# Kernel optimization log

Hardware: AMD Instinct MI355X
Metric: run time of the kernel (lower is better)

Reference implementation:

```python
import jax, jax.numpy as jnp
import numpy as np

N = 50000
E = 800000
D_IN, D_HID, D_OUT = 128, 128, 64


def setup_inputs() -> dict:
    key = jax.random.key(0)
    ks = jax.random.split(key, 8)
    x = jax.random.normal(ks[0], (N, D_IN), dtype=jnp.float32)
    edge_index = jax.random.randint(ks[1], (2, E), 0, N, dtype=jnp.int64)
    # Glorot-ish init for GCNConv linear weights + zero bias (PyG default bias=True)
    def lin(k, din, dout):
        s = 1.0 / np.sqrt(din)
        return jax.random.uniform(k, (din, dout), jnp.float32, -s, s)
    return {
        "x": x,
        "edge_index": edge_index,
        "W1": lin(ks[2], D_IN, D_HID), "b1": jnp.zeros((D_HID,), jnp.float32),
        "W2": lin(ks[3], D_HID, D_HID), "b2": jnp.zeros((D_HID,), jnp.float32),
        "W3": lin(ks[4], D_HID, D_OUT), "b3": jnp.zeros((D_OUT,), jnp.float32),
    }


def _prep_edges(edge_index, n):
    # add self loops (PyG GCNConv default add_self_loops=True)
    loop = jnp.arange(n, dtype=edge_index.dtype)
    src = jnp.concatenate([edge_index[0], loop])
    dst = jnp.concatenate([edge_index[1], loop])
    deg = jax.ops.segment_sum(jnp.ones_like(dst, dtype=jnp.float32), dst, num_segments=n)
    dinv = jnp.where(deg > 0, jax.lax.rsqrt(deg), 0.0)
    norm = dinv[src] * dinv[dst]  # symmetric normalization per edge
    return src, dst, norm


def _gcn_conv(h, W, b, src, dst, norm, n):
    h = h @ W                                   # [N, dout]
    msg = h[src] * norm[:, None]                # [E+N, dout] gather
    out = jax.ops.segment_sum(msg, dst, num_segments=n)  # scatter-add
    return out + b


def reference(x, edge_index, W1, b1, W2, b2, W3, b3):
    src, dst, norm = _prep_edges(edge_index, N)
    h = jax.nn.relu(_gcn_conv(x, W1, b1, src, dst, norm, N))
    h = jax.nn.relu(_gcn_conv(h, W2, b2, src, dst, norm, N))
    return _gcn_conv(h, W3, b3, src, dst, norm, N)  # eval mode: dropout is identity
```

## Files before the change

kernel.cpp:

```cpp
#include <hip/hip_runtime.h>
#include <hip/hip_fp16.h>
#include <math.h>

#define NN 50000
#define NE 800000
#define RAWSTRIDE 96
#define NBUCK 196
#define NBBIN 196
#define BCAP 4608
#define ACH 4096
#define G1B 782
#define G2B 1563

using bf8v = __attribute__((ext_vector_type(8))) short;
using f4v  = __attribute__((ext_vector_type(4))) float;

__device__ inline unsigned short f2bf(float f) {
    unsigned int u = __float_as_uint(f);
    u += 0x7FFFu + ((u >> 16) & 1u);
    return (unsigned short)(u >> 16);
}
__device__ inline float bflo(unsigned int d) { return __uint_as_float(d << 16); }
__device__ inline float bfhi(unsigned int d) { return __uint_as_float(d & 0xFFFF0000u); }


__global__ __launch_bounds__(256) void prep_kernel(const float* __restrict__ W1,
                                                   const float* __restrict__ W2,
                                                   unsigned int* __restrict__ w1p,
                                                   unsigned int* __restrict__ w2p,
                                                   int* __restrict__ gcursor) {
    int id = blockIdx.x * 256 + threadIdx.x;
    int m = id >> 13;
    int rest = id & 8191;
    int n = rest >> 6;
    int kp = rest & 63;
    int k = kp * 2;
    const float* W = m ? W2 : W1;
    unsigned int* o = m ? w2p : w1p;
    unsigned int p = (unsigned int)f2bf(W[k * 128 + n]) |
                     ((unsigned int)f2bf(W[(k + 1) * 128 + n]) << 16);
    o[n * 64 + kp] = p;
    if (id < NBUCK) gcursor[id] = 0;
}


__device__ __forceinline__ void bin_body(const int* __restrict__ src,
                                         const int* __restrict__ dst,
                                         int* __restrict__ gcursor,
                                         unsigned int* __restrict__ bst,
                                         int bx, char* shc) {
    unsigned int* items = (unsigned int*)shc;
    int* cnt    = (int*)(shc + 16384);
    int* pref   = (int*)(shc + 17408);
    int* gstart = (int*)(shc + 18436);
    const int t = threadIdx.x;
    cnt[t] = 0;
    __syncthreads();
    const int base = bx * ACH;

    unsigned int my[16]; int myb[16], myr[16];
    #pragma unroll
    for (int i = 0; i < 16; ++i) {
        int e = base + i * 256 + t;
        my[i] = 0; myb[i] = -1; myr[i] = 0;
        if (e < NE) {
            int d = dst[e], s = src[e];
            my[i] = (unsigned int)s | ((unsigned int)d << 16);
            int b = d >> 8;
            myb[i] = b;
            myr[i] = atomicAdd(&cnt[b], 1);
        }
    }
    __syncthreads();
    if (t == 0) {
        int run = 0;
        for (int b = 0; b < 256; ++b) { pref[b] = run; run += cnt[b]; }
        pref[256] = run;
    }
    __syncthreads();
    if (cnt[t] > 0) gstart[t] = atomicAdd(&gcursor[t], cnt[t]);
    __syncthreads();
    #pragma unroll
    for (int i = 0; i < 16; ++i)
        if (myb[i] >= 0) items[pref[myb[i]] + myr[i]] = my[i];
    __syncthreads();
    const int total = pref[256];
    for (int i = t; i < total; i += 256) {
        int lo = 0, hi = 255;
        while (lo < hi) { int mid = (lo + hi + 1) >> 1; if (pref[mid] <= i) lo = mid; else hi = mid - 1; }
        int idx = gstart[lo] + (i - pref[lo]);
        if (idx < BCAP) bst[(size_t)lo * BCAP + idx] = items[i];
    }
}


__global__ __launch_bounds__(512) void sortb_kernel(const int* __restrict__ gcursor,
                                                    const unsigned int* __restrict__ bst,
                                                    int* __restrict__ cnt_g,
                                                    float* __restrict__ dinv,
                                                    unsigned short* __restrict__ raw) {
    __shared__ unsigned int items[BCAP];
    __shared__ int cnt[256], pref[257], cur[256];
    __shared__ unsigned short outl[BCAP];
    const int b = blockIdx.x;
    const int t = threadIdx.x;
    int n = gcursor[b];
    if (n > BCAP) n = BCAP;
    if (t < 256) { cnt[t] = 0; cur[t] = 0; }
    __syncthreads();
    for (int i = t; i < n; i += 512) {
        unsigned int u = bst[(size_t)b * BCAP + i];
        items[i] = u;
        atomicAdd(&cnt[(u >> 16) & 255], 1);
    }
    __syncthreads();
    if (t == 0) {
        int run = 0;
        for (int j = 0; j < 256; ++j) { pref[j] = run; run += cnt[j]; }
        pref[256] = run;
    }
    __syncthreads();
    for (int i = t; i < n; i += 512) {
        unsigned int u = items[i];
        int ln = (u >> 16) & 255;
        int r = atomicAdd(&cur[ln], 1);
        outl[pref[ln] + r] = (unsigned short)(u & 0xFFFFu);
    }
    __syncthreads();
    for (int i = t; i < n; i += 512) {
        int lo = 0, hi = 255;
        while (lo < hi) { int mid = (lo + hi + 1) >> 1; if (pref[mid] <= i) lo = mid; else hi = mid - 1; }
        int r = i - pref[lo];
        if (r < RAWSTRIDE) raw[(size_t)(b * 256 + lo) * RAWSTRIDE + r] = outl[i];
    }
    if (t < 256) {
        int node = b * 256 + t;
        if (node < NN) {
            int c = cnt[t];
            cnt_g[node] = c;
            dinv[node] = rsqrtf((float)(1 + c));
        }
    }
}


__device__ __forceinline__ void gemm128_body_f32(const float* __restrict__ A,
                                                 const unsigned short* __restrict__ Wbf,
                                                 unsigned short* __restrict__ out,
                                                 int bx, char* shc) {
    unsigned short* Dt = (unsigned short*)shc;
    const int t = threadIdx.x;
    const int row0 = bx * 64;
    const int wave = t >> 6;
    const int l64  = t & 63;
    const int m16  = l64 & 15;
    const int quad = l64 >> 4;
    const int arow = row0 + wave * 16 + m16;
    const int arowc = (arow < NN) ? arow : 0;

    f4v acc[8];
    #pragma unroll
    for (int i = 0; i < 8; ++i) acc[i] = (f4v)(0.0f);

    #pragma unroll
    for (int k0 = 0; k0 < 128; k0 += 32) {
        bf8v afrag;
        const float4* ap = (const float4*)(A + (size_t)arowc * 128 + k0 + quad * 8);
        float4 a0 = ap[0], a1 = ap[1];
        afrag[0] = (short)f2bf(a0.x); afrag[1] = (short)f2bf(a0.y);
        afrag[2] = (short)f2bf(a0.z); afrag[3] = (short)f2bf(a0.w);
        afrag[4] = (short)f2bf(a1.x); afrag[5] = (short)f2bf(a1.y);
        afrag[6] = (short)f2bf(a1.z); afrag[7] = (short)f2bf(a1.w);
        #pragma unroll
        for (int nt = 0; nt < 8; ++nt) {
            bf8v bfrag = *(const bf8v*)(Wbf + (nt * 16 + m16) * 128 + k0 + quad * 8);
            acc[nt] = __builtin_amdgcn_mfma_f32_16x16x32_bf16(afrag, bfrag, acc[nt], 0, 0, 0);
        }
    }

    #pragma unroll
    for (int nt = 0; nt < 8; ++nt) {
        #pragma unroll
        for (int r = 0; r < 4; ++r) {
            Dt[(wave * 16 + quad * 4 + r) * 136 + nt * 16 + m16] = f2bf(acc[nt][r]);
        }
    }
    __syncthreads();

    #pragma unroll
    for (int j = 0; j < 4; ++j) {
        int idx = j * 256 + t;
        int r = idx >> 4, c4 = idx & 15;
        int gr = row0 + r;
        if (gr < NN)
            ((uint4*)(out + (size_t)gr * 128))[c4] = ((const uint4*)&Dt[r * 136])[c4];
    }
}

__global__ __launch_bounds__(256) void bin_g1_kernel(const int* __restrict__ src,
                                                     const int* __restrict__ dst,
                                                     int* __restrict__ gcursor,
                                                     unsigned int* __restrict__ bst,
                                                     const float* __restrict__ x,
                                                     const unsigned short* __restrict__ w1bf,
                                                     unsigned short* __restrict__ hb) {
    __shared__ __align__(16) char sh[19472];
    if (blockIdx.x < NBBIN) {
        bin_body(src, dst, gcursor, bst, blockIdx.x, sh);
    } else {
        gemm128_body_f32(x, w1bf, hb, blockIdx.x - NBBIN, sh);
    }
}


#define ACC8(G, W_) \
    acc[0] += W_ * bflo(G.x); acc[1] += W_ * bfhi(G.x); \
    acc[2] += W_ * bflo(G.y); acc[3] += W_ * bfhi(G.y); \
    acc[4] += W_ * bflo(G.z); acc[5] += W_ * bfhi(G.z); \
    acc[6] += W_ * bflo(G.w); acc[7] += W_ * bfhi(G.w);

#define AGG128_BODY(HV, RROW, C, DIW, LANE)                                         \
    {                                                                               \
        uint4 g = HV[(size_t)wid * 16 + (LANE)];                                    \
        float ws = (DIW) * (DIW);                                                   \
        acc[0] = ws * bflo(g.x); acc[1] = ws * bfhi(g.x);                           \
        acc[2] = ws * bflo(g.y); acc[3] = ws * bfhi(g.y);                           \
        acc[4] = ws * bflo(g.z); acc[5] = ws * bfhi(g.z);                           \
        acc[6] = ws * bflo(g.w); acc[7] = ws * bfhi(g.w);                           \
    }                                                                               \
    const int cfull = (C) & ~7;                                                     \
    uint4 q;                                                                        \
    if (cfull > 0) q = *(const uint4*)(RROW);                                       \
    for (int e = 0; e < cfull; e += 8) {                                            \
        uint4 qc = q;                                                               \
        if (e + 8 < cfull) q = *(const uint4*)((RROW) + e + 8);                     \
        int c0 = qc.x & 0xFFFFu, c1 = qc.x >> 16;                                   \
        int c2 = qc.y & 0xFFFFu, c3 = qc.y >> 16;                                   \
        int c4 = qc.z & 0xFFFFu, c5 = qc.z >> 16;                                   \
        int c6 = qc.w & 0xFFFFu, c7 = qc.w >> 16;                                   \
        uint4 g0 = HV[(size_t)c0 * 16 + (LANE)];                                    \
        uint4 g1 = HV[(size_t)c1 * 16 + (LANE)];                                    \
        uint4 g2 = HV[(size_t)c2 * 16 + (LANE)];                                    \
        uint4 g3 = HV[(size_t)c3 * 16 + (LANE)];                                    \
        uint4 g4 = HV[(size_t)c4 * 16 + (LANE)];                                    \
        uint4 g5 = HV[(size_t)c5 * 16 + (LANE)];                                    \
        uint4 g6 = HV[(size_t)c6 * 16 + (LANE)];                                    \
        uint4 g7 = HV[(size_t)c7 * 16 + (LANE)];                                    \
        float w0 = (DIW) * dinv[c0], w1 = (DIW) * dinv[c1];                         \
        float w2 = (DIW) * dinv[c2], w3 = (DIW) * dinv[c3];                         \
        float w4 = (DIW) * dinv[c4], w5 = (DIW) * dinv[c5];                         \
        float w6 = (DIW) * dinv[c6], w7 = (DIW) * dinv[c7];                         \
        ACC8(g0, w0) ACC8(g1, w1) ACC8(g2, w2) ACC8(g3, w3)                         \
        ACC8(g4, w4) ACC8(g5, w5) ACC8(g6, w6) ACC8(g7, w7)                         \
    }                                                                               \
    if ((C) & 7) {                                                                  \
        int e = cfull, rem = (C) - e;                                               \
        uint4 qc = *(const uint4*)((RROW) + e);                                     \
        int c0 = qc.x & 0xFFFFu, c1 = qc.x >> 16;                                   \
        int c2 = qc.y & 0xFFFFu, c3 = qc.y >> 16;                                   \
        int c4 = qc.z & 0xFFFFu, c5 = qc.z >> 16;                                   \
        int c6 = qc.w & 0xFFFFu, c7 = qc.w >> 16;                                   \
        if (rem <= 1) c1 = 0; if (rem <= 2) c2 = 0; if (rem <= 3) c3 = 0;           \
        if (rem <= 4) c4 = 0; if (rem <= 5) c5 = 0; if (rem <= 6) c6 = 0;           \
        c7 = 0;                                                                     \
        float w0 = (DIW) * dinv[c0];                                                \
        float w1 = (rem > 1) ? (DIW) * dinv[c1] : 0.f;                              \
        float w2 = (rem > 2) ? (DIW) * dinv[c2] : 0.f;                              \
        float w3 = (rem > 3) ? (DIW) * dinv[c3] : 0.f;                              \
        float w4 = (rem > 4) ? (DIW) * dinv[c4] : 0.f;                              \
        float w5 = (rem > 5) ? (DIW) * dinv[c5] : 0.f;                              \
        float w6 = (rem > 6) ? (DIW) * dinv[c6] : 0.f;                              \
        float w7 = 0.f;                                                             \
        uint4 g0 = HV[(size_t)c0 * 16 + (LANE)];                                    \
        uint4 g1 = HV[(size_t)c1 * 16 + (LANE)];                                    \
        uint4 g2 = HV[(size_t)c2 * 16 + (LANE)];                                    \
        uint4 g3 = HV[(size_t)c3 * 16 + (LANE)];                                    \
        uint4 g4 = HV[(size_t)c4 * 16 + (LANE)];                                    \
        uint4 g5 = HV[(size_t)c5 * 16 + (LANE)];                                    \
        uint4 g6 = HV[(size_t)c6 * 16 + (LANE)];                                    \
        uint4 g7 = HV[(size_t)c7 * 16 + (LANE)];                                    \
        ACC8(g0, w0) ACC8(g1, w1) ACC8(g2, w2) ACC8(g3, w3)                         \
        ACC8(g4, w4) ACC8(g5, w5) ACC8(g6, w6) ACC8(g7, w7)                         \
    }


__global__ __launch_bounds__(256) void aggW2_kernel(const unsigned short* __restrict__ hin,
                                                    const unsigned short* __restrict__ raw,
                                                    const int* __restrict__ cnt_g,
                                                    const float* __restrict__ dinv,
                                                    const float* __restrict__ bias,
                                                    const unsigned short* __restrict__ Wbf,
                                                    unsigned short* __restrict__ out) {
    __shared__ unsigned short Zt[32 * 136];
    const int t = threadIdx.x;
    const int row0 = blockIdx.x * 32;
    const int group = t >> 4;
    const int lane  = t & 15;
    const uint4* hv = (const uint4*)hin;
    const float4* bp = (const float4*)bias;
    float4 bv0 = bp[lane * 2], bv1 = bp[lane * 2 + 1];

    for (int r = 0; r < 2; ++r) {
        const int wid = row0 + r * 16 + group;
        uint4 o = make_uint4(0u, 0u, 0u, 0u);
        if (wid < NN) {
            int c = cnt_g[wid];
            if (c > RAWSTRIDE) c = RAWSTRIDE;
            const float diw = dinv[wid];
            const unsigned short* rrow = raw + (size_t)wid * RAWSTRIDE;
            float acc[8];
            AGG128_BODY(hv, rrow, c, diw, lane)
            acc[0] += bv0.x; acc[1] += bv0.y; acc[2] += bv0.z; acc[3] += bv0.w;
            acc[4] += bv1.x; acc[5] += bv1.y; acc[6] += bv1.z; acc[7] += bv1.w;
            #pragma unroll
            for (int j = 0; j < 8; ++j) acc[j] = fmaxf(acc[j], 0.f);
            o.x = (unsigned int)f2bf(acc[0]) | ((unsigned int)f2bf(acc[1]) << 16);
            o.y = (unsigned int)f2bf(acc[2]) | ((unsigned int)f2bf(acc[3]) << 16);
            o.z = (unsigned int)f2bf(acc[4]) | ((unsigned int)f2bf(acc[5]) << 16);
            o.w = (unsigned int)f2bf(acc[6]) | ((unsigned int)f2bf(acc[7]) << 16);
        }
        *(uint4*)&Zt[(r * 16 + group) * 136 + lane * 8] = o;
    }
    __syncthreads();

    const int wave = t >> 6;
    const int l64  = t & 63;
    const int m16  = l64 & 15;
    const int quad = l64 >> 4;
    const int rh = wave & 1;
    const int nh = wave >> 1;

    f4v acc[4];
    #pragma unroll
    for (int i = 0; i < 4; ++i) acc[i] = (f4v)(0.0f);

    #pragma unroll
    for (int k0 = 0; k0 < 128; k0 += 32) {
        bf8v afrag = *(const bf8v*)&Zt[(rh * 16 + m16) * 136 + k0 + quad * 8];
        #pragma unroll
        for (int j = 0; j < 4; ++j) {
            int nt = nh * 4 + j;
            bf8v bfrag = *(const bf8v*)(Wbf + (nt * 16 + m16) * 128 + k0 + quad * 8);
            acc[j] = __builtin_amdgcn_mfma_f32_16x16x32_bf16(afrag, bfrag, acc[j], 0, 0, 0);
        }
    }
    __syncthreads();

    #pragma unroll
    for (int j = 0; j < 4; ++j) {
        #pragma unroll
        for (int rr = 0; rr < 4; ++rr) {
            Zt[(rh * 16 + quad * 4 + rr) * 136 + (nh * 4 + j) * 16 + m16] = f2bf(acc[j][rr]);
        }
    }
    __syncthreads();

    #pragma unroll
    for (int jj = 0; jj < 2; ++jj) {
        int idx = jj * 256 + t;
        int r = idx >> 4, c4 = idx & 15;
        int gr = row0 + r;
        if (gr < NN)
            ((uint4*)(out + (size_t)gr * 128))[c4] = ((const uint4*)&Zt[r * 136])[c4];
    }
}


__global__ __launch_bounds__(256) void aggG3_kernel(const unsigned short* __restrict__ hin,
                                                    const unsigned short* __restrict__ raw,
                                                    const int* __restrict__ cnt_g,
                                                    const float* __restrict__ dinv,
                                                    const float* __restrict__ bias,
                                                    const float* __restrict__ W,
                                                    unsigned short* __restrict__ outh) {
    __shared__ unsigned short Zt[32 * 136];
    const int t = threadIdx.x;
    const int row0 = blockIdx.x * 32;
    const int group = t >> 4;
    const int lane  = t & 15;
    const uint4* hv = (const uint4*)hin;
    const float4* bp = (const float4*)bias;
    float4 bv0 = bp[lane * 2], bv1 = bp[lane * 2 + 1];

    for (int r = 0; r < 2; ++r) {
        const int wid = row0 + r * 16 + group;
        uint4 o = make_uint4(0u, 0u, 0u, 0u);
        if (wid < NN) {
            int c = cnt_g[wid];
            if (c > RAWSTRIDE) c = RAWSTRIDE;
            const float diw = dinv[wid];
            const unsigned short* rrow = raw + (size_t)wid * RAWSTRIDE;
            float acc[8];
            AGG128_BODY(hv, rrow, c, diw, lane)
            acc[0] += bv0.x; acc[1] += bv0.y; acc[2] += bv0.z; acc[3] += bv0.w;
            acc[4] += bv1.x; acc[5] += bv1.y; acc[6] += bv1.z; acc[7] += bv1.w;
            #pragma unroll
            for (int j = 0; j < 8; ++j) acc[j] = fmaxf(acc[j], 0.f);
            o.x = (unsigned int)f2bf(acc[0]) | ((unsigned int)f2bf(acc[1]) << 16);
            o.y = (unsigned int)f2bf(acc[2]) | ((unsigned int)f2bf(acc[3]) << 16);
            o.z = (unsigned int)f2bf(acc[4]) | ((unsigned int)f2bf(acc[5]) << 16);
            o.w = (unsigned int)f2bf(acc[6]) | ((unsigned int)f2bf(acc[7]) << 16);
        }
        *(uint4*)&Zt[(r * 16 + group) * 136 + lane * 8] = o;
    }
    __syncthreads();

    const int cg = t & 15;
    const int rt = t >> 4;
    const float4* Wv = (const float4*)W;
    float4 acc[2];
    acc[0] = make_float4(0.f, 0.f, 0.f, 0.f);
    acc[1] = make_float4(0.f, 0.f, 0.f, 0.f);

    for (int k0 = 0; k0 < 128; k0 += 4) {
        float4 w0 = Wv[(k0 + 0) * 16 + cg];
        float4 w1 = Wv[(k0 + 1) * 16 + cg];
        float4 w2 = Wv[(k0 + 2) * 16 + cg];
        float4 w3 = Wv[(k0 + 3) * 16 + cg];
        #pragma unroll
        for (int i = 0; i < 2; ++i) {
            uint2 u = *(const uint2*)&Zt[(rt * 2 + i) * 136 + k0];
            float ax = bflo(u.x), ay = bfhi(u.x), az = bflo(u.y), aw = bfhi(u.y);
            acc[i].x += ax * w0.x + ay * w1.x + az * w2.x + aw * w3.x;
            acc[i].y += ax * w0.y + ay * w1.y + az * w2.y + aw * w3.y;
            acc[i].z += ax * w0.z + ay * w1.z + az * w2.z + aw * w3.z;
            acc[i].w += ax * w0.w + ay * w1.w + az * w2.w + aw * w3.w;
        }
    }

    #pragma unroll
    for (int i = 0; i < 2; ++i) {
        int gr = row0 + rt * 2 + i;
        if (gr < NN) {
            uint2 o;
            o.x = (unsigned int)f2bf(acc[i].x) | ((unsigned int)f2bf(acc[i].y) << 16);
            o.y = (unsigned int)f2bf(acc[i].z) | ((unsigned int)f2bf(acc[i].w) << 16);
            ((uint2*)(outh + (size_t)gr * 64))[cg] = o;
        }
    }
}


__global__ __launch_bounds__(256) void agg3_kernel(const unsigned short* __restrict__ hin,
                                                   const unsigned short* __restrict__ raw,
                                                   const int* __restrict__ cnt_g,
                                                   const float* __restrict__ dinv,
                                                   const float* __restrict__ bias,
                                                   float* __restrict__ out) {
    const int t = threadIdx.x;
    const int group = t >> 3;
    const int lane  = t & 7;
    const int wid = blockIdx.x * 32 + group;
    if (wid >= NN) return;

    int c = cnt_g[wid];
    if (c > RAWSTRIDE) c = RAWSTRIDE;
    const float diw = dinv[wid];
    const unsigned short* rrow = raw + (size_t)wid * RAWSTRIDE;
    const uint4* hv = (const uint4*)hin;

    float acc[8];
    {
        uint4 g = hv[(size_t)wid * 8 + lane];
        float ws = diw * diw;
        acc[0] = ws * bflo(g.x); acc[1] = ws * bfhi(g.x);
        acc[2] = ws * bflo(g.y); acc[3] = ws * bfhi(g.y);
        acc[4] = ws * bflo(g.z); acc[5] = ws * bfhi(g.z);
        acc[6] = ws * bflo(g.w); acc[7] = ws * bfhi(g.w);
    }

    const int cfull = c & ~7;
    uint4 q;
    if (cfull > 0) q = *(const uint4*)(rrow);
    for (int e = 0; e < cfull; e += 8) {
        uint4 qc = q;
        if (e + 8 < cfull) q = *(const uint4*)(rrow + e + 8);
        int c0 = qc.x & 0xFFFFu, c1 = qc.x >> 16;
        int c2 = qc.y & 0xFFFFu, c3 = qc.y >> 16;
        int c4 = qc.z & 0xFFFFu, c5 = qc.z >> 16;
        int c6 = qc.w & 0xFFFFu, c7 = qc.w >> 16;
        uint4 g0 = hv[(size_t)c0 * 8 + lane];
        uint4 g1 = hv[(size_t)c1 * 8 + lane];
        uint4 g2 = hv[(size_t)c2 * 8 + lane];
        uint4 g3 = hv[(size_t)c3 * 8 + lane];
        uint4 g4 = hv[(size_t)c4 * 8 + lane];
        uint4 g5 = hv[(size_t)c5 * 8 + lane];
        uint4 g6 = hv[(size_t)c6 * 8 + lane];
        uint4 g7 = hv[(size_t)c7 * 8 + lane];
        float w0 = diw * dinv[c0], w1 = diw * dinv[c1];
        float w2 = diw * dinv[c2], w3 = diw * dinv[c3];
        float w4 = diw * dinv[c4], w5 = diw * dinv[c5];
        float w6 = diw * dinv[c6], w7 = diw * dinv[c7];
        ACC8(g0, w0) ACC8(g1, w1) ACC8(g2, w2) ACC8(g3, w3)
        ACC8(g4, w4) ACC8(g5, w5) ACC8(g6, w6) ACC8(g7, w7)
    }
    if (c & 7) {
        int e = cfull, rem = c - e;
        uint4 qc = *(const uint4*)(rrow + e);
        int c0 = qc.x & 0xFFFFu, c1 = qc.x >> 16;
        int c2 = qc.y & 0xFFFFu, c3 = qc.y >> 16;
        int c4 = qc.z & 0xFFFFu, c5 = qc.z >> 16;
        int c6 = qc.w & 0xFFFFu, c7 = qc.w >> 16;
        if (rem <= 1) c1 = 0; if (rem <= 2) c2 = 0; if (rem <= 3) c3 = 0;
        if (rem <= 4) c4 = 0; if (rem <= 5) c5 = 0; if (rem <= 6) c6 = 0;
        c7 = 0;
        float w0 = diw * dinv[c0];
        float w1 = (rem > 1) ? diw * dinv[c1] : 0.f;
        float w2 = (rem > 2) ? diw * dinv[c2] : 0.f;
        float w3 = (rem > 3) ? diw * dinv[c3] : 0.f;
        float w4 = (rem > 4) ? diw * dinv[c4] : 0.f;
        float w5 = (rem > 5) ? diw * dinv[c5] : 0.f;
        float w6 = (rem > 6) ? diw * dinv[c6] : 0.f;
        float w7 = 0.f;
        uint4 g0 = hv[(size_t)c0 * 8 + lane];
        uint4 g1 = hv[(size_t)c1 * 8 + lane];
        uint4 g2 = hv[(size_t)c2 * 8 + lane];
        uint4 g3 = hv[(size_t)c3 * 8 + lane];
        uint4 g4 = hv[(size_t)c4 * 8 + lane];
        uint4 g5 = hv[(size_t)c5 * 8 + lane];
        uint4 g6 = hv[(size_t)c6 * 8 + lane];
        uint4 g7 = hv[(size_t)c7 * 8 + lane];
        ACC8(g0, w0) ACC8(g1, w1) ACC8(g2, w2) ACC8(g3, w3)
        ACC8(g4, w4) ACC8(g5, w5) ACC8(g6, w6) ACC8(g7, w7)
    }

    const float4* bp = (const float4*)bias;
    float4 b0 = bp[lane * 2], b1 = bp[lane * 2 + 1];
    acc[0] += b0.x; acc[1] += b0.y; acc[2] += b0.z; acc[3] += b0.w;
    acc[4] += b1.x; acc[5] += b1.y; acc[6] += b1.z; acc[7] += b1.w;

    float4 o0 = make_float4(acc[0], acc[1], acc[2], acc[3]);
    float4 o1 = make_float4(acc[4], acc[5], acc[6], acc[7]);
    ((float4*)(out + (size_t)wid * 64))[lane * 2]     = o0;
    ((float4*)(out + (size_t)wid * 64))[lane * 2 + 1] = o1;
}


extern "C" void kernel_launch(void* const* d_in, const int* in_sizes, int n_in,
                              void* d_out, int out_size, void* d_ws, size_t ws_size,
                              hipStream_t stream) {
    const float* x  = (const float*)d_in[0];
    const int*   ei = (const int*)d_in[1];
    const float* W1 = (const float*)d_in[2];
    const float* b1 = (const float*)d_in[3];
    const float* W2 = (const float*)d_in[4];
    const float* b2 = (const float*)d_in[5];
    const float* W3 = (const float*)d_in[6];
    const float* b3 = (const float*)d_in[7];
    float* out = (float*)d_out;

    char* w = (char*)d_ws;
    int*   cnt_g   = (int*)  (w + 0x0000000);
    int*   gcursor = (int*)  (w + 0x0040000);
    float* dinv    = (float*)(w + 0x0048000);
    unsigned int*   w1p = (unsigned int*)  (w + 0x0080000);
    unsigned int*   w2p = (unsigned int*)  (w + 0x0088000);
    unsigned int*   bst = (unsigned int*)  (w + 0x0090000);
    unsigned short* raw = (unsigned short*)(w + 0x0480000);
    unsigned short* hb  = (unsigned short*)(w + 0x0E00000);
    unsigned short* h2b = (unsigned short*)(w + 0x1B00000);
    unsigned short* h3b = (unsigned short*)(w + 0x2800000);

    const int* src = ei;
    const int* dst = ei + NE;

    prep_kernel<<<64, 256, 0, stream>>>(W1, W2, w1p, w2p, gcursor);
    bin_g1_kernel<<<NBBIN + G1B, 256, 0, stream>>>(src, dst, gcursor, bst, x,
                                                   (const unsigned short*)w1p, hb);
    sortb_kernel<<<NBUCK, 512, 0, stream>>>(gcursor, bst, cnt_g, dinv, raw);
    aggW2_kernel<<<G2B, 256, 0, stream>>>(hb, raw, cnt_g, dinv, b1,
                                          (const unsigned short*)w2p, h2b);
    aggG3_kernel<<<G2B, 256, 0, stream>>>(h2b, raw, cnt_g, dinv, b2, W3, h3b);
    agg3_kernel<<<(NN + 31) / 32, 256, 0, stream>>>(h3b, raw, cnt_g, dinv, b3, out);
}
```

Before: 245.0 us.

## Split feature dims into column slabs for L2-resident gathers, unfuse GEMMs

Node feature matrices are stored in column-slab layout (32-column bf16 slabs), and aggregation kernels are launched per slab so each gather touches a smaller working set that can stay in cache. The fused aggregate+GEMM kernels are split into a generic templated slab aggregation kernel plus separate GEMM kernels for layers 2 and 3. This adds extra launches and a round trip of intermediate activations through memory, and each gather now moves 4 bytes per lane instead of 16, which may raise instruction overhead.

```diff
diff --git a/kernel.cpp b/kernel.cpp
--- a/kernel.cpp
+++ b/kernel.cpp
@@ -9,8 +9,7 @@
 #define NBBIN 196
 #define BCAP 4608
 #define ACH 4096
-#define G1B 782
-#define G2B 1563
+#define NBS 782
 
 using bf8v = __attribute__((ext_vector_type(8))) short;
 using f4v  = __attribute__((ext_vector_type(4))) float;
@@ -187,13 +186,15 @@
     }
     __syncthreads();
 
+    uint4* ou4 = (uint4*)out;
     #pragma unroll
     for (int j = 0; j < 4; ++j) {
         int idx = j * 256 + t;
         int r = idx >> 4, c4 = idx & 15;
         int gr = row0 + r;
         if (gr < NN)
-            ((uint4*)(out + (size_t)gr * 128))[c4] = ((const uint4*)&Dt[r * 136])[c4];
+            ou4[(size_t)(c4 >> 2) * NN * 4 + (size_t)gr * 4 + (c4 & 3)] =
+                ((const uint4*)&Dt[r * 136])[c4];
     }
 }
 
@@ -213,113 +214,131 @@
 }
 
 
-#define ACC8(G, W_) \
-    acc[0] += W_ * bflo(G.x); acc[1] += W_ * bfhi(G.x); \
-    acc[2] += W_ * bflo(G.y); acc[3] += W_ * bfhi(G.y); \
-    acc[4] += W_ * bflo(G.z); acc[5] += W_ * bfhi(G.z); \
-    acc[6] += W_ * bflo(G.w); acc[7] += W_ * bfhi(G.w);
-
-#define AGG128_BODY(HV, RROW, C, DIW, LANE)                                         \
-    {                                                                               \
-        uint4 g = HV[(size_t)wid * 16 + (LANE)];                                    \
-        float ws = (DIW) * (DIW);                                                   \
-        acc[0] = ws * bflo(g.x); acc[1] = ws * bfhi(g.x);                           \
-        acc[2] = ws * bflo(g.y); acc[3] = ws * bfhi(g.y);                           \
-        acc[4] = ws * bflo(g.z); acc[5] = ws * bfhi(g.z);                           \
-        acc[6] = ws * bflo(g.w); acc[7] = ws * bfhi(g.w);                           \
-    }                                                                               \
-    const int cfull = (C) & ~7;                                                     \
-    uint4 q;                                                                        \
-    if (cfull > 0) q = *(const uint4*)(RROW);                                       \
-    for (int e = 0; e < cfull; e += 8) {                                            \
-        uint4 qc = q;                                                               \
-        if (e + 8 < cfull) q = *(const uint4*)((RROW) + e + 8);                     \
-        int c0 = qc.x & 0xFFFFu, c1 = qc.x >> 16;                                   \
-        int c2 = qc.y & 0xFFFFu, c3 = qc.y >> 16;                                   \
-        int c4 = qc.z & 0xFFFFu, c5 = qc.z >> 16;                                   \
-        int c6 = qc.w & 0xFFFFu, c7 = qc.w >> 16;                                   \
-        uint4 g0 = HV[(size_t)c0 * 16 + (LANE)];                                    \
-        uint4 g1 = HV[(size_t)c1 * 16 + (LANE)];                                    \
-        uint4 g2 = HV[(size_t)c2 * 16 + (LANE)];                                    \
-        uint4 g3 = HV[(size_t)c3 * 16 + (LANE)];                                    \
-        uint4 g4 = HV[(size_t)c4 * 16 + (LANE)];                                    \
-        uint4 g5 = HV[(size_t)c5 * 16 + (LANE)];                                    \
-        uint4 g6 = HV[(size_t)c6 * 16 + (LANE)];                                    \
-        uint4 g7 = HV[(size_t)c7 * 16 + (LANE)];                                    \
-        float w0 = (DIW) * dinv[c0], w1 = (DIW) * dinv[c1];                         \
-        float w2 = (DIW) * dinv[c2], w3 = (DIW) * dinv[c3];                         \
-        float w4 = (DIW) * dinv[c4], w5 = (DIW) * dinv[c5];                         \
-        float w6 = (DIW) * dinv[c6], w7 = (DIW) * dinv[c7];                         \
-        ACC8(g0, w0) ACC8(g1, w1) ACC8(g2, w2) ACC8(g3, w3)                         \
-        ACC8(g4, w4) ACC8(g5, w5) ACC8(g6, w6) ACC8(g7, w7)                         \
-    }                                                                               \
-    if ((C) & 7) {                                                                  \
-        int e = cfull, rem = (C) - e;                                               \
-        uint4 qc = *(const uint4*)((RROW) + e);                                     \
-        int c0 = qc.x & 0xFFFFu, c1 = qc.x >> 16;                                   \
-        int c2 = qc.y & 0xFFFFu, c3 = qc.y >> 16;                                   \
-        int c4 = qc.z & 0xFFFFu, c5 = qc.z >> 16;                                   \
-        int c6 = qc.w & 0xFFFFu, c7 = qc.w >> 16;                                   \
-        if (rem <= 1) c1 = 0; if (rem <= 2) c2 = 0; if (rem <= 3) c3 = 0;           \
-        if (rem <= 4) c4 = 0; if (rem <= 5) c5 = 0; if (rem <= 6) c6 = 0;           \
-        c7 = 0;                                                                     \
-        float w0 = (DIW) * dinv[c0];                                                \
-        float w1 = (rem > 1) ? (DIW) * dinv[c1] : 0.f;                              \
-        float w2 = (rem > 2) ? (DIW) * dinv[c2] : 0.f;                              \
-        float w3 = (rem > 3) ? (DIW) * dinv[c3] : 0.f;                              \
-        float w4 = (rem > 4) ? (DIW) * dinv[c4] : 0.f;                              \
-        float w5 = (rem > 5) ? (DIW) * dinv[c5] : 0.f;                              \
-        float w6 = (rem > 6) ? (DIW) * dinv[c6] : 0.f;                              \
-        float w7 = 0.f;                                                             \
-        uint4 g0 = HV[(size_t)c0 * 16 + (LANE)];                                    \
-        uint4 g1 = HV[(size_t)c1 * 16 + (LANE)];                                    \
-        uint4 g2 = HV[(size_t)c2 * 16 + (LANE)];                                    \
-        uint4 g3 = HV[(size_t)c3 * 16 + (LANE)];                                    \
-        uint4 g4 = HV[(size_t)c4 * 16 + (LANE)];                                    \
-        uint4 g5 = HV[(size_t)c5 * 16 + (LANE)];                                    \
-        uint4 g6 = HV[(size_t)c6 * 16 + (LANE)];                                    \
-        uint4 g7 = HV[(size_t)c7 * 16 + (LANE)];                                    \
-        ACC8(g0, w0) ACC8(g1, w1) ACC8(g2, w2) ACC8(g3, w3)                         \
-        ACC8(g4, w4) ACC8(g5, w5) ACC8(g6, w6) ACC8(g7, w7)                         \
-    }
-
-
-__global__ __launch_bounds__(256) void aggW2_kernel(const unsigned short* __restrict__ hin,
+template <bool RELU, bool OUTF32>
+__global__ __launch_bounds__(256) void aggst_kernel(const unsigned short* __restrict__ hin,
                                                     const unsigned short* __restrict__ raw,
                                                     const int* __restrict__ cnt_g,
                                                     const float* __restrict__ dinv,
                                                     const float* __restrict__ bias,
-                                                    const unsigned short* __restrict__ Wbf,
-                                                    unsigned short* __restrict__ out) {
-    __shared__ unsigned short Zt[32 * 136];
-    const int t = threadIdx.x;
-    const int row0 = blockIdx.x * 32;
+                                                    void* __restrict__ outv) {
+    const int t = threadIdx.x;
+    const int s   = blockIdx.x / NBS;
+    const int blk = blockIdx.x % NBS;
+    const int row0 = blk * 64;
     const int group = t >> 4;
     const int lane  = t & 15;
-    const uint4* hv = (const uint4*)hin;
-    const float4* bp = (const float4*)bias;
-    float4 bv0 = bp[lane * 2], bv1 = bp[lane * 2 + 1];
-
-    for (int r = 0; r < 2; ++r) {
+    const unsigned int* hvS = (const unsigned int*)hin + (size_t)s * NN * 16;
+    const float2 bb = ((const float2*)bias)[s * 16 + lane];
+
+    for (int r = 0; r < 4; ++r) {
         const int wid = row0 + r * 16 + group;
-        uint4 o = make_uint4(0u, 0u, 0u, 0u);
-        if (wid < NN) {
-            int c = cnt_g[wid];
-            if (c > RAWSTRIDE) c = RAWSTRIDE;
-            const float diw = dinv[wid];
-            const unsigned short* rrow = raw + (size_t)wid * RAWSTRIDE;
-            float acc[8];
-            AGG128_BODY(hv, rrow, c, diw, lane)
-            acc[0] += bv0.x; acc[1] += bv0.y; acc[2] += bv0.z; acc[3] += bv0.w;
-            acc[4] += bv1.x; acc[5] += bv1.y; acc[6] += bv1.z; acc[7] += bv1.w;
-            #pragma unroll
-            for (int j = 0; j < 8; ++j) acc[j] = fmaxf(acc[j], 0.f);
-            o.x = (unsigned int)f2bf(acc[0]) | ((unsigned int)f2bf(acc[1]) << 16);
-            o.y = (unsigned int)f2bf(acc[2]) | ((unsigned int)f2bf(acc[3]) << 16);
-            o.z = (unsigned int)f2bf(acc[4]) | ((unsigned int)f2bf(acc[5]) << 16);
-            o.w = (unsigned int)f2bf(acc[6]) | ((unsigned int)f2bf(acc[7]) << 16);
-        }
-        *(uint4*)&Zt[(r * 16 + group) * 136 + lane * 8] = o;
+        if (wid >= NN) continue;
+        int c = cnt_g[wid];
+        if (c > RAWSTRIDE) c = RAWSTRIDE;
+        const float diw = dinv[wid];
+        const unsigned short* rrow = raw + (size_t)wid * RAWSTRIDE;
+
+        float a0, a1;
+        {
+            unsigned int g = hvS[(size_t)wid * 16 + lane];
+            float ws = diw * diw;
+            a0 = ws * bflo(g); a1 = ws * bfhi(g);
+        }
+
+        const int cfull = c & ~7;
+        uint4 q;
+        if (cfull > 0) q = *(const uint4*)(rrow);
+        for (int e = 0; e < cfull; e += 8) {
+            uint4 qc = q;
+            if (e + 8 < cfull) q = *(const uint4*)(rrow + e + 8);
+            int c0 = qc.x & 0xFFFFu, c1 = qc.x >> 16;
+            int c2 = qc.y & 0xFFFFu, c3 = qc.y >> 16;
+            int c4 = qc.z & 0xFFFFu, c5 = qc.z >> 16;
+            int c6 = qc.w & 0xFFFFu, c7 = qc.w >> 16;
+            unsigned int g0 = hvS[(size_t)c0 * 16 + lane];
+            unsigned int g1 = hvS[(size_t)c1 * 16 + lane];
+            unsigned int g2 = hvS[(size_t)c2 * 16 + lane];
+            unsigned int g3 = hvS[(size_t)c3 * 16 + lane];
+            unsigned int g4 = hvS[(size_t)c4 * 16 + lane];
+            unsigned int g5 = hvS[(size_t)c5 * 16 + lane];
+            unsigned int g6 = hvS[(size_t)c6 * 16 + lane];
+            unsigned int g7 = hvS[(size_t)c7 * 16 + lane];
+            float w0 = diw * dinv[c0], w1 = diw * dinv[c1];
+            float w2 = diw * dinv[c2], w3 = diw * dinv[c3];
+            float w4 = diw * dinv[c4], w5 = diw * dinv[c5];
+            float w6 = diw * dinv[c6], w7 = diw * dinv[c7];
+            a0 += w0 * bflo(g0); a1 += w0 * bfhi(g0);
+            a0 += w1 * bflo(g1); a1 += w1 * bfhi(g1);
+            a0 += w2 * bflo(g2); a1 += w2 * bfhi(g2);
+            a0 += w3 * bflo(g3); a1 += w3 * bfhi(g3);
+            a0 += w4 * bflo(g4); a1 += w4 * bfhi(g4);
+            a0 += w5 * bflo(g5); a1 += w5 * bfhi(g5);
+            a0 += w6 * bflo(g6); a1 += w6 * bfhi(g6);
+            a0 += w7 * bflo(g7); a1 += w7 * bfhi(g7);
+        }
+        if (c & 7) {
+            int e = cfull, rem = c - e;
+            uint4 qc = *(const uint4*)(rrow + e);
+            int c0 = qc.x & 0xFFFFu, c1 = qc.x >> 16;
+            int c2 = qc.y & 0xFFFFu, c3 = qc.y >> 16;
+            int c4 = qc.z & 0xFFFFu, c5 = qc.z >> 16;
+            int c6 = qc.w & 0xFFFFu, c7 = qc.w >> 16;
+            if (rem <= 1) c1 = 0; if (rem <= 2) c2 = 0; if (rem <= 3) c3 = 0;
+            if (rem <= 4) c4 = 0; if (rem <= 5) c5 = 0; if (rem <= 6) c6 = 0;
+            c7 = 0;
+            float w0 = diw * dinv[c0];
+            float w1 = (rem > 1) ? diw * dinv[c1] : 0.f;
+            float w2 = (rem > 2) ? diw * dinv[c2] : 0.f;
+            float w3 = (rem > 3) ? diw * dinv[c3] : 0.f;
+            float w4 = (rem > 4) ? diw * dinv[c4] : 0.f;
+            float w5 = (rem > 5) ? diw * dinv[c5] : 0.f;
+            float w6 = (rem > 6) ? diw * dinv[c6] : 0.f;
+            unsigned int g0 = hvS[(size_t)c0 * 16 + lane];
+            unsigned int g1 = hvS[(size_t)c1 * 16 + lane];
+            unsigned int g2 = hvS[(size_t)c2 * 16 + lane];
+            unsigned int g3 = hvS[(size_t)c3 * 16 + lane];
+            unsigned int g4 = hvS[(size_t)c4 * 16 + lane];
+            unsigned int g5 = hvS[(size_t)c5 * 16 + lane];
+            unsigned int g6 = hvS[(size_t)c6 * 16 + lane];
+            a0 += w0 * bflo(g0); a1 += w0 * bfhi(g0);
+            a0 += w1 * bflo(g1); a1 += w1 * bfhi(g1);
+            a0 += w2 * bflo(g2); a1 += w2 * bfhi(g2);
+            a0 += w3 * bflo(g3); a1 += w3 * bfhi(g3);
+            a0 += w4 * bflo(g4); a1 += w4 * bfhi(g4);
+            a0 += w5 * bflo(g5); a1 += w5 * bfhi(g5);
+            a0 += w6 * bflo(g6); a1 += w6 * bfhi(g6);
+        }
+
+        a0 += bb.x; a1 += bb.y;
+        if (RELU) { a0 = fmaxf(a0, 0.f); a1 = fmaxf(a1, 0.f); }
+        if (OUTF32) {
+            float* o = (float*)outv;
+            *(float2*)&o[(size_t)wid * 64 + s * 32 + lane * 2] = make_float2(a0, a1);
+        } else {
+            unsigned int* zo = (unsigned int*)outv + (size_t)s * NN * 16;
+            zo[(size_t)wid * 16 + lane] =
+                (unsigned int)f2bf(a0) | ((unsigned int)f2bf(a1) << 16);
+        }
+    }
+}
+
+
+__global__ __launch_bounds__(256) void gemm2_kernel(const unsigned short* __restrict__ z1,
+                                                    const unsigned short* __restrict__ Wbf,
+                                                    unsigned short* __restrict__ h2) {
+    __shared__ __align__(16) unsigned short At[64 * 136];
+    const int t = threadIdx.x;
+    const int row0 = blockIdx.x * 64;
+    const uint4* zu4 = (const uint4*)z1;
+
+    #pragma unroll
+    for (int j = 0; j < 4; ++j) {
+        int idx = j * 256 + t;
+        int r = idx >> 4, c4 = idx & 15;
+        int gr = row0 + r;
+        uint4 v = make_uint4(0u, 0u, 0u, 0u);
+        if (gr < NN) v = zu4[(size_t)(c4 >> 2) * NN * 4 + (size_t)gr * 4 + (c4 & 3)];
+        *(uint4*)&At[r * 136 + c4 * 8] = v;
     }
     __syncthreads();
 
@@ -327,212 +346,102 @@
     const int l64  = t & 63;
     const int m16  = l64 & 15;
     const int quad = l64 >> 4;
-    const int rh = wave & 1;
-    const int nh = wave >> 1;
-
-    f4v acc[4];
-    #pragma unroll
-    for (int i = 0; i < 4; ++i) acc[i] = (f4v)(0.0f);
+
+    f4v acc[8];
+    #pragma unroll
+    for (int i = 0; i < 8; ++i) acc[i] = (f4v)(0.0f);
 
     #pragma unroll
     for (int k0 = 0; k0 < 128; k0 += 32) {
-        bf8v afrag = *(const bf8v*)&Zt[(rh * 16 + m16) * 136 + k0 + quad * 8];
+        bf8v afrag = *(const bf8v*)&At[(wave * 16 + m16) * 136 + k0 + quad * 8];
         #pragma unroll
-        for (int j = 0; j < 4; ++j) {
-            int nt = nh * 4 + j;
+        for (int nt = 0; nt < 8; ++nt) {
             bf8v bfrag = *(const bf8v*)(Wbf + (nt * 16 + m16) * 128 + k0 + quad * 8);
-            acc[j] = __builtin_amdgcn_mfma_f32_16x16x32_bf16(afrag, bfrag, acc[j], 0, 0, 0);
-        }
-    }
-    __syncthreads();
-
+            acc[nt] = __builtin_amdgcn_mfma_f32_16x16x32_bf16(afrag, bfrag, acc[nt], 0, 0, 0);
+        }
+    }
+    __syncthreads();
+
+    #pragma unroll
+    for (int nt = 0; nt < 8; ++nt) {
+        #pragma unroll
+        for (int r = 0; r < 4; ++r) {
+            At[(wave * 16 + quad * 4 + r) * 136 + nt * 16 + m16] = f2bf(acc[nt][r]);
+        }
+    }
+    __syncthreads();
+
+    uint4* ou4 = (uint4*)h2;
     #pragma unroll
     for (int j = 0; j < 4; ++j) {
-        #pragma unroll
-        for (int rr = 0; rr < 4; ++rr) {
-            Zt[(rh * 16 + quad * 4 + rr) * 136 + (nh * 4 + j) * 16 + m16] = f2bf(acc[j][rr]);
-        }
-    }
-    __syncthreads();
-
-    #pragma unroll
-    for (int jj = 0; jj < 2; ++jj) {
-        int idx = jj * 256 + t;
+        int idx = j * 256 + t;
         int r = idx >> 4, c4 = idx & 15;
         int gr = row0 + r;
         if (gr < NN)
-            ((uint4*)(out + (size_t)gr * 128))[c4] = ((const uint4*)&Zt[r * 136])[c4];
-    }
-}
-
-
-__global__ __launch_bounds__(256) void aggG3_kernel(const unsigned short* __restrict__ hin,
-                                                    const unsigned short* __restrict__ raw,
-                                                    const int* __restrict__ cnt_g,
-                                                    const float* __restrict__ dinv,
-                                                    const float* __restrict__ bias,
+            ou4[(size_t)(c4 >> 2) * NN * 4 + (size_t)gr * 4 + (c4 & 3)] =
+                ((const uint4*)&At[r * 136])[c4];
+    }
+}
+
+
+__global__ __launch_bounds__(256) void gemm3_kernel(const unsigned short* __restrict__ z2,
                                                     const float* __restrict__ W,
-                                                    unsigned short* __restrict__ outh) {
-    __shared__ unsigned short Zt[32 * 136];
-    const int t = threadIdx.x;
-    const int row0 = blockIdx.x * 32;
-    const int group = t >> 4;
-    const int lane  = t & 15;
-    const uint4* hv = (const uint4*)hin;
-    const float4* bp = (const float4*)bias;
-    float4 bv0 = bp[lane * 2], bv1 = bp[lane * 2 + 1];
-
-    for (int r = 0; r < 2; ++r) {
-        const int wid = row0 + r * 16 + group;
-        uint4 o = make_uint4(0u, 0u, 0u, 0u);
-        if (wid < NN) {
-            int c = cnt_g[wid];
-            if (c > RAWSTRIDE) c = RAWSTRIDE;
-            const float diw = dinv[wid];
-            const unsigned short* rrow = raw + (size_t)wid * RAWSTRIDE;
-            float acc[8];
-            AGG128_BODY(hv, rrow, c, diw, lane)
-            acc[0] += bv0.x; acc[1] += bv0.y; acc[2] += bv0.z; acc[3] += bv0.w;
-            acc[4] += bv1.x; acc[5] += bv1.y; acc[6] += bv1.z; acc[7] += bv1.w;
-            #pragma unroll
-            for (int j = 0; j < 8; ++j) acc[j] = fmaxf(acc[j], 0.f);
-            o.x = (unsigned int)f2bf(acc[0]) | ((unsigned int)f2bf(acc[1]) << 16);
-            o.y = (unsigned int)f2bf(acc[2]) | ((unsigned int)f2bf(acc[3]) << 16);
-            o.z = (unsigned int)f2bf(acc[4]) | ((unsigned int)f2bf(acc[5]) << 16);
-            o.w = (unsigned int)f2bf(acc[6]) | ((unsigned int)f2bf(acc[7]) << 16);
-        }
-        *(uint4*)&Zt[(r * 16 + group) * 136 + lane * 8] = o;
-    }
-    __syncthreads();
-
-    const int cg = t & 15;
-    const int rt = t >> 4;
+                                                    unsigned short* __restrict__ h3) {
+    constexpr int LD = 132;
+    __shared__ float lds[64 * LD];
+    const int t = threadIdx.x;
+    const int row0 = blockIdx.x * 64;
+    const uint2* zu2 = (const uint2*)z2;
+
+    #pragma unroll
+    for (int j = 0; j < 8; ++j) {
+        int idx = j * 256 + t;
+        int r = idx >> 5, c4 = idx & 31;
+        int gr = row0 + r;
+        uint2 u = make_uint2(0u, 0u);
+        if (gr < NN) u = zu2[(size_t)(c4 >> 3) * NN * 8 + (size_t)gr * 8 + (c4 & 7)];
+        float4 v;
+        v.x = bflo(u.x); v.y = bfhi(u.x); v.z = bflo(u.y); v.w = bfhi(u.y);
+        ((float4*)(lds + r * LD))[c4] = v;
+    }
+    __syncthreads();
+
+    constexpr int CG = 16;
+    constexpr int RPT = 4;
+    const int cg = t % CG;
+    const int rt = t / CG;
     const float4* Wv = (const float4*)W;
-    float4 acc[2];
-    acc[0] = make_float4(0.f, 0.f, 0.f, 0.f);
-    acc[1] = make_float4(0.f, 0.f, 0.f, 0.f);
+    float4 acc[RPT];
+    #pragma unroll
+    for (int i = 0; i < RPT; ++i) acc[i] = make_float4(0.f, 0.f, 0.f, 0.f);
 
     for (int k0 = 0; k0 < 128; k0 += 4) {
-        float4 w0 = Wv[(k0 + 0) * 16 + cg];
-        float4 w1 = Wv[(k0 + 1) * 16 + cg];
-        float4 w2 = Wv[(k0 + 2) * 16 + cg];
-        float4 w3 = Wv[(k0 + 3) * 16 + cg];
+        float4 w0 = Wv[(k0 + 0) * CG + cg];
+        float4 w1 = Wv[(k0 + 1) * CG + cg];
+        float4 w2 = Wv[(k0 + 2) * CG + cg];
+        float4 w3 = Wv[(k0 + 3) * CG + cg];
         #pragma unroll
-        for (int i = 0; i < 2; ++i) {
-            uint2 u = *(const uint2*)&Zt[(rt * 2 + i) * 136 + k0];
-            float ax = bflo(u.x), ay = bfhi(u.x), az = bflo(u.y), aw = bfhi(u.y);
-            acc[i].x += ax * w0.x + ay * w1.x + az * w2.x + aw * w3.x;
-            acc[i].y += ax * w0.y + ay * w1.y + az * w2.y + aw * w3.y;
-            acc[i].z += ax * w0.z + ay * w1.z + az * w2.z + aw * w3.z;
-            acc[i].w += ax * w0.w + ay * w1.w + az * w2.w + aw * w3.w;
-        }
-    }
-
-    #pragma unroll
-    for (int i = 0; i < 2; ++i) {
-        int gr = row0 + rt * 2 + i;
+        for (int i = 0; i < RPT; ++i) {
+            const float* lr = lds + (rt * RPT + i) * LD;
+            float4 a = ((const float4*)lr)[k0 >> 2];
+            acc[i].x += a.x * w0.x + a.y * w1.x + a.z * w2.x + a.w * w3.x;
+            acc[i].y += a.x * w0.y + a.y * w1.y + a.z * w2.y + a.w * w3.y;
+            acc[i].z += a.x * w0.z + a.y * w1.z + a.z * w2.z + a.w * w3.z;
+            acc[i].w += a.x * w0.w + a.y * w1.w + a.z * w2.w + a.w * w3.w;
+        }
+    }
+
+    uint2* ou2 = (uint2*)h3;
+    #pragma unroll
+    for (int i = 0; i < RPT; ++i) {
+        int gr = row0 + rt * RPT + i;
         if (gr < NN) {
             uint2 o;
             o.x = (unsigned int)f2bf(acc[i].x) | ((unsigned int)f2bf(acc[i].y) << 16);
             o.y = (unsigned int)f2bf(acc[i].z) | ((unsigned int)f2bf(acc[i].w) << 16);
-            ((uint2*)(outh + (size_t)gr * 64))[cg] = o;
-        }
-    }
-}
-
-
-__global__ __launch_bounds__(256) void agg3_kernel(const unsigned short* __restrict__ hin,
-                                                   const unsigned short* __restrict__ raw,
-                                                   const int* __restrict__ cnt_g,
-                                                   const float* __restrict__ dinv,
-                                                   const float* __restrict__ bias,
-                                                   float* __restrict__ out) {
-    const int t = threadIdx.x;
-    const int group = t >> 3;
-    const int lane  = t & 7;
-    const int wid = blockIdx.x * 32 + group;
-    if (wid >= NN) return;
-
-    int c = cnt_g[wid];
-    if (c > RAWSTRIDE) c = RAWSTRIDE;
-    const float diw = dinv[wid];
-    const unsigned short* rrow = raw + (size_t)wid * RAWSTRIDE;
-    const uint4* hv = (const uint4*)hin;
-
-    float acc[8];
-    {
-        uint4 g = hv[(size_t)wid * 8 + lane];
-        float ws = diw * diw;
-        acc[0] = ws * bflo(g.x); acc[1] = ws * bfhi(g.x);
-        acc[2] = ws * bflo(g.y); acc[3] = ws * bfhi(g.y);
-        acc[4] = ws * bflo(g.z); acc[5] = ws * bfhi(g.z);
-        acc[6] = ws * bflo(g.w); acc[7] = ws * bfhi(g.w);
-    }
-
-    const int cfull = c & ~7;
-    uint4 q;
-    if (cfull > 0) q = *(const uint4*)(rrow);
-    for (int e = 0; e < cfull; e += 8) {
-        uint4 qc = q;
-        if (e + 8 < cfull) q = *(const uint4*)(rrow + e + 8);
-        int c0 = qc.x & 0xFFFFu, c1 = qc.x >> 16;
-        int c2 = qc.y & 0xFFFFu, c3 = qc.y >> 16;
-        int c4 = qc.z & 0xFFFFu, c5 = qc.z >> 16;
-        int c6 = qc.w & 0xFFFFu, c7 = qc.w >> 16;
-        uint4 g0 = hv[(size_t)c0 * 8 + lane];
-        uint4 g1 = hv[(size_t)c1 * 8 + lane];
-        uint4 g2 = hv[(size_t)c2 * 8 + lane];
-        uint4 g3 = hv[(size_t)c3 * 8 + lane];
-        uint4 g4 = hv[(size_t)c4 * 8 + lane];
-        uint4 g5 = hv[(size_t)c5 * 8 + lane];
-        uint4 g6 = hv[(size_t)c6 * 8 + lane];
-        uint4 g7 = hv[(size_t)c7 * 8 + lane];
-        float w0 = diw * dinv[c0], w1 = diw * dinv[c1];
-        float w2 = diw * dinv[c2], w3 = diw * dinv[c3];
-        float w4 = diw * dinv[c4], w5 = diw * dinv[c5];
-        float w6 = diw * dinv[c6], w7 = diw * dinv[c7];
-        ACC8(g0, w0) ACC8(g1, w1) ACC8(g2, w2) ACC8(g3, w3)
-        ACC8(g4, w4) ACC8(g5, w5) ACC8(g6, w6) ACC8(g7, w7)
-    }
-    if (c & 7) {
-        int e = cfull, rem = c - e;
-        uint4 qc = *(const uint4*)(rrow + e);
-        int c0 = qc.x & 0xFFFFu, c1 = qc.x >> 16;
-        int c2 = qc.y & 0xFFFFu, c3 = qc.y >> 16;
-        int c4 = qc.z & 0xFFFFu, c5 = qc.z >> 16;
-        int c6 = qc.w & 0xFFFFu, c7 = qc.w >> 16;
-        if (rem <= 1) c1 = 0; if (rem <= 2) c2 = 0; if (rem <= 3) c3 = 0;
-        if (rem <= 4) c4 = 0; if (rem <= 5) c5 = 0; if (rem <= 6) c6 = 0;
-        c7 = 0;
-        float w0 = diw * dinv[c0];
-        float w1 = (rem > 1) ? diw * dinv[c1] : 0.f;
-        float w2 = (rem > 2) ? diw * dinv[c2] : 0.f;
-        float w3 = (rem > 3) ? diw * dinv[c3] : 0.f;
-        float w4 = (rem > 4) ? diw * dinv[c4] : 0.f;
-        float w5 = (rem > 5) ? diw * dinv[c5] : 0.f;
-        float w6 = (rem > 6) ? diw * dinv[c6] : 0.f;
-        float w7 = 0.f;
-        uint4 g0 = hv[(size_t)c0 * 8 + lane];
-        uint4 g1 = hv[(size_t)c1 * 8 + lane];
-        uint4 g2 = hv[(size_t)c2 * 8 + lane];
-        uint4 g3 = hv[(size_t)c3 * 8 + lane];
-        uint4 g4 = hv[(size_t)c4 * 8 + lane];
-        uint4 g5 = hv[(size_t)c5 * 8 + lane];
-        uint4 g6 = hv[(size_t)c6 * 8 + lane];
-        uint4 g7 = hv[(size_t)c7 * 8 + lane];
-        ACC8(g0, w0) ACC8(g1, w1) ACC8(g2, w2) ACC8(g3, w3)
-        ACC8(g4, w4) ACC8(g5, w5) ACC8(g6, w6) ACC8(g7, w7)
-    }
-
-    const float4* bp = (const float4*)bias;
-    float4 b0 = bp[lane * 2], b1 = bp[lane * 2 + 1];
-    acc[0] += b0.x; acc[1] += b0.y; acc[2] += b0.z; acc[3] += b0.w;
-    acc[4] += b1.x; acc[5] += b1.y; acc[6] += b1.z; acc[7] += b1.w;
-
-    float4 o0 = make_float4(acc[0], acc[1], acc[2], acc[3]);
-    float4 o1 = make_float4(acc[4], acc[5], acc[6], acc[7]);
-    ((float4*)(out + (size_t)wid * 64))[lane * 2]     = o0;
-    ((float4*)(out + (size_t)wid * 64))[lane * 2 + 1] = o1;
+            ou2[(size_t)(cg >> 3) * NN * 8 + (size_t)gr * 8 + (cg & 7)] = o;
+        }
+    }
 }
 
 
@@ -557,19 +466,20 @@
     unsigned int*   w2p = (unsigned int*)  (w + 0x0088000);
     unsigned int*   bst = (unsigned int*)  (w + 0x0090000);
     unsigned short* raw = (unsigned short*)(w + 0x0480000);
-    unsigned short* hb  = (unsigned short*)(w + 0x0E00000);
-    unsigned short* h2b = (unsigned short*)(w + 0x1B00000);
-    unsigned short* h3b = (unsigned short*)(w + 0x2800000);
+    unsigned short* hbuf  = (unsigned short*)(w + 0x0E00000);
+    unsigned short* zbuf  = (unsigned short*)(w + 0x1B00000);
+    unsigned short* h3buf = (unsigned short*)(w + 0x2800000);
 
     const int* src = ei;
     const int* dst = ei + NE;
 
     prep_kernel<<<64, 256, 0, stream>>>(W1, W2, w1p, w2p, gcursor);
-    bin_g1_kernel<<<NBBIN + G1B, 256, 0, stream>>>(src, dst, gcursor, bst, x,
-                                                   (const unsigned short*)w1p, hb);
+    bin_g1_kernel<<<NBBIN + NBS, 256, 0, stream>>>(src, dst, gcursor, bst, x,
+                                                   (const unsigned short*)w1p, hbuf);
     sortb_kernel<<<NBUCK, 512, 0, stream>>>(gcursor, bst, cnt_g, dinv, raw);
-    aggW2_kernel<<<G2B, 256, 0, stream>>>(hb, raw, cnt_g, dinv, b1,
-                                          (const unsigned short*)w2p, h2b);
-    aggG3_kernel<<<G2B, 256, 0, stream>>>(h2b, raw, cnt_g, dinv, b2, W3, h3b);
-    agg3_kernel<<<(NN + 31) / 32, 256, 0, stream>>>(h3b, raw, cnt_g, dinv, b3, out);
-}
+    aggst_kernel<true, false><<<4 * NBS, 256, 0, stream>>>(hbuf, raw, cnt_g, dinv, b1, zbuf);
+    gemm2_kernel<<<NBS, 256, 0, stream>>>(zbuf, (const unsigned short*)w2p, hbuf);
+    aggst_kernel<true, false><<<4 * NBS, 256, 0, stream>>>(hbuf, raw, cnt_g, dinv, b2, zbuf);
+    gemm3_kernel<<<NBS, 256, 0, stream>>>(zbuf, W3, h3buf);
+    aggst_kernel<false, true><<<2 * NBS, 256, 0, stream>>>(h3buf, raw, cnt_g, dinv, b3, out);
+}
```

New measurement: 297.8 us. +21.5%, slower.
